# Kernel optimization log

Hardware: AMD Instinct MI355X
Metric: run time of the kernel (lower is better)

The kernel has to match this reference:

```python
import jax, jax.numpy as jnp
import numpy as np


def setup_inputs() -> dict:
    key = jax.random.key(0)
    k_x, k_wxh, k_whh, k_fcw, k_fcb = jax.random.split(key, 5)
    B, T, I, H = 256, 512, 64, 512
    x = jax.random.normal(k_x, (B, T, I), dtype=jnp.float32)
    W_xh = jax.random.normal(k_wxh, (I, H), dtype=jnp.float32) * 0.01
    W_hh = jax.random.normal(k_whh, (H, H), dtype=jnp.float32) * 0.01
    b = jnp.zeros((H,), dtype=jnp.float32)
    # nn.Linear(H, 1): weight (1, H), bias (1); init ~ U(-1/sqrt(H), 1/sqrt(H))
    lim = 1.0 / np.sqrt(H)
    fc_w = jax.random.uniform(k_fcw, (1, H), dtype=jnp.float32, minval=-lim, maxval=lim)
    fc_b = jax.random.uniform(k_fcb, (1,), dtype=jnp.float32, minval=-lim, maxval=lim)
    return {"x": x, "W_xh": W_xh, "W_hh": W_hh, "b": b, "fc_w": fc_w, "fc_b": fc_b}


def reference(x, W_xh, W_hh, b, fc_w, fc_b):
    B, T, I = x.shape
    H = W_hh.shape[0]
    # Precompute input projections for all timesteps in one big matmul: (B,T,H)
    xh = jnp.einsum('bti,ih->bth', x, W_xh) + b
    h0 = jnp.zeros((B, H), dtype=x.dtype)

    def step(h, xh_t):
        h_new = jnp.tanh(xh_t + h @ W_hh)
        return h_new, None

    h_final, _ = jax.lax.scan(step, h0, jnp.swapaxes(xh, 0, 1))  # scan over T
    return h_final @ fc_w.T + fc_b  # (B, 1)
```

## Files before the change

kernel.cpp:

```cpp
#include <hip/hip_runtime.h>


#define BATCH    256
#define TSTEPS   512
#define IDIM     64
#define HDIM     512
#define NTH      512

typedef _Float16 half2_t __attribute__((ext_vector_type(2)));
typedef _Float16 half8_t __attribute__((ext_vector_type(8)));

union H8U {
    half8_t v;
    half2_t p[4];
    uint4   u4;
};

__device__ __forceinline__ float fdot2(half2_t a, half2_t b, float c) {
#if __has_builtin(__builtin_amdgcn_fdot2)
    return __builtin_amdgcn_fdot2(a, b, c, false);
#else
    return c + (float)a[0] * (float)b[0] + (float)a[1] * (float)b[1];
#endif
}

__device__ __forceinline__ float fast_tanh(float x) {
    float e = __builtin_amdgcn_exp2f(x * 2.88539008177792681472f);
    return 1.0f - 2.0f * __builtin_amdgcn_rcpf(e + 1.0f);
}

#define XH_ROWS 16
__global__ __launch_bounds__(NTH, 4)
void xh_gemm(const float* __restrict__ x, const float* __restrict__ Wxh,
             const float* __restrict__ bias, _Float16* __restrict__ xh)
{
    const int j = threadIdx.x;
    const size_t r0 = (size_t)blockIdx.x * XH_ROWS;
    float wcol[IDIM];
#pragma unroll
    for (int i = 0; i < IDIM; ++i) wcol[i] = Wxh[(size_t)i * HDIM + j];
    const float bj = bias[j];
#pragma unroll
    for (int r = 0; r < XH_ROWS; ++r) {
        const float* xr = x + (r0 + r) * IDIM;
        float acc = bj;
#pragma unroll
        for (int i = 0; i < IDIM; ++i) acc += xr[i] * wcol[i];
        xh[(r0 + r) * HDIM + j] = (_Float16)acc;
    }
}

#define S_RP   192
#define S_RC   48
#define S_LC   16
#define S_LSTR 17
#define S_LDSW_BYTES (512 * S_LSTR * 16)
#define S_HBUF_OFF   S_LDSW_BYTES
#define S_HBUF_ELEMS 512
#define S_RED_OFF    (S_HBUF_OFF + 2 * S_HBUF_ELEMS * 2)
#define S_SMEM_BYTES (S_RED_OFF + 64)

__global__ __attribute__((amdgpu_flat_work_group_size(NTH, NTH), amdgpu_waves_per_eu(2, 2)))
void rnn_split(const _Float16* __restrict__ xh,
               const float* __restrict__ Whh,
               const float* __restrict__ fcw,
               const float* __restrict__ fcb,
               float* __restrict__ out)
{
    extern __shared__ char smem[];
    uint4*    ldsW = reinterpret_cast<uint4*>(smem);
    _Float16* hbuf = reinterpret_cast<_Float16*>(smem + S_HBUF_OFF);
    float*    red  = reinterpret_cast<float*>(smem + S_RED_OFF);

    const int j = threadIdx.x;
    const int b = blockIdx.x;

    half2_t wreg[S_RP];
#pragma unroll
    for (int p = 0; p < S_RP; ++p) {
        const int k = 2 * p;
        half2_t w;
        w[0] = (_Float16)Whh[(size_t)k * HDIM + j];
        w[1] = (_Float16)Whh[(size_t)(k + 1) * HDIM + j];
        wreg[p] = w;
    }
#pragma unroll
    for (int cc = 0; cc < S_LC; ++cc) {
        H8U u;
#pragma unroll
        for (int q = 0; q < 4; ++q) {
            const int k0 = 384 + 8 * cc + 2 * q;
            half2_t w;
            w[0] = (_Float16)Whh[(size_t)k0 * HDIM + j];
            w[1] = (_Float16)Whh[(size_t)(k0 + 1) * HDIM + j];
            u.p[q] = w;
        }
        ldsW[j * S_LSTR + cc] = u.u4;
    }

    const float fcwj = fcw[j];
    const _Float16* xhb = xh + (size_t)b * TSTEPS * HDIM;

    hbuf[j] = (_Float16)0.0f;
    __syncthreads();

    float hval = 0.0f;
    for (int t = 0; t < TSTEPS; ++t) {
        const int cur = t & 1;
        const int nxt = cur ^ 1;
        const _Float16* hb = hbuf + cur * S_HBUF_ELEMS;

        const float xv = (float)xhb[(size_t)t * HDIM + j];

        float a0 = 0.0f, a1 = 0.0f, a2 = 0.0f, a3 = 0.0f;
#pragma unroll
        for (int c = 0; c < S_RC; ++c) {
            H8U u;
            u.v = *reinterpret_cast<const half8_t*>(hb + 8 * c);
            a0 = fdot2(u.p[0], wreg[4 * c + 0], a0);
            a1 = fdot2(u.p[1], wreg[4 * c + 1], a1);
            a2 = fdot2(u.p[2], wreg[4 * c + 2], a2);
            a3 = fdot2(u.p[3], wreg[4 * c + 3], a3);
        }
#pragma unroll
        for (int cc = 0; cc < S_LC; ++cc) {
            H8U u, w;
            u.v  = *reinterpret_cast<const half8_t*>(hb + 8 * (S_RC + cc));
            w.u4 = ldsW[j * S_LSTR + cc];
            a0 = fdot2(u.p[0], w.p[0], a0);
            a1 = fdot2(u.p[1], w.p[1], a1);
            a2 = fdot2(u.p[2], w.p[2], a2);
            a3 = fdot2(u.p[3], w.p[3], a3);
        }
        hval = fast_tanh(((a0 + a1) + (a2 + a3)) + xv);

        hbuf[nxt * S_HBUF_ELEMS + j] = (_Float16)hval;
        __syncthreads();
    }

    float partial = hval * fcwj;
#pragma unroll
    for (int off = 32; off >= 1; off >>= 1)
        partial += __shfl_down(partial, off, 64);
    if ((j & 63) == 0) red[j >> 6] = partial;
    __syncthreads();
    if (j == 0) {
        float s = 0.0f;
#pragma unroll
        for (int w = 0; w < 8; ++w) s += red[w];
        out[b] = s + fcb[0];
    }
}

#define F_RP   216
#define F_RC   54
#define F_LC   18
#define F_LSTR 19
#define F_LDSW_BYTES (512 * F_LSTR * 16)
#define F_HBUF_OFF   F_LDSW_BYTES
#define F_HBUF_ELEMS 640
#define F_RED_OFF    (F_HBUF_OFF + 2 * F_HBUF_ELEMS * 2)
#define F_SMEM_BYTES (F_RED_OFF + 64)

__global__ __attribute__((amdgpu_flat_work_group_size(NTH, NTH), amdgpu_waves_per_eu(2, 2)))
void rnn_fused(const float* __restrict__ x, const float* __restrict__ Wxh,
               const float* __restrict__ Whh, const float* __restrict__ bias,
               const float* __restrict__ fcw, const float* __restrict__ fcb,
               float* __restrict__ out)
{
    extern __shared__ char smem[];
    uint4*    ldsW = reinterpret_cast<uint4*>(smem);
    _Float16* hbuf = reinterpret_cast<_Float16*>(smem + F_HBUF_OFF);
    float*    red  = reinterpret_cast<float*>(smem + F_RED_OFF);

    const int j = threadIdx.x;
    const int b = blockIdx.x;

    half2_t wreg[F_RP];
#pragma unroll
    for (int p = 0; p < F_RP; ++p) {
        const int k = 2 * p;
        half2_t w;
        w[0] = (_Float16)Whh[(size_t)k * HDIM + j];
        w[1] = (_Float16)Whh[(size_t)(k + 1) * HDIM + j];
        wreg[p] = w;
    }
#pragma unroll
    for (int cc = 0; cc < F_LC; ++cc) {
        H8U u;
#pragma unroll
        for (int q = 0; q < 4; ++q) {
            const int k0 = 432 + 8 * cc + 2 * q;
            const int k1 = k0 + 1;
            half2_t w;
            w[0] = (_Float16)(k0 < HDIM ? Whh[(size_t)k0 * HDIM + j]
                                        : Wxh[(size_t)(k0 - HDIM) * HDIM + j]);
            w[1] = (_Float16)(k1 < HDIM ? Whh[(size_t)k1 * HDIM + j]
                                        : Wxh[(size_t)(k1 - HDIM) * HDIM + j]);
            u.p[q] = w;
        }
        ldsW[j * F_LSTR + cc] = u.u4;
    }

    const float bj   = bias[j];
    const float fcwj = fcw[j];

    hbuf[j] = (_Float16)0.0f;
    if (j < IDIM) hbuf[HDIM + j] = (_Float16)x[((size_t)b * TSTEPS + 0) * IDIM + j];
    __syncthreads();

    float hval = 0.0f;
    for (int t = 0; t < TSTEPS; ++t) {
        const int cur = t & 1;
        const int nxt = cur ^ 1;
        const _Float16* hb = hbuf + cur * F_HBUF_ELEMS;

        float xv = 0.0f;
        const bool do_x = (j < IDIM) && (t + 1 < TSTEPS);
        if (do_x) xv = x[((size_t)b * TSTEPS + (t + 1)) * IDIM + j];

        float a0 = bj, a1 = 0.0f, a2 = 0.0f, a3 = 0.0f;
#pragma unroll
        for (int c = 0; c < F_RC; ++c) {
            H8U u;
            u.v = *reinterpret_cast<const half8_t*>(hb + 8 * c);
            a0 = fdot2(u.p[0], wreg[4 * c + 0], a0);
            a1 = fdot2(u.p[1], wreg[4 * c + 1], a1);
            a2 = fdot2(u.p[2], wreg[4 * c + 2], a2);
            a3 = fdot2(u.p[3], wreg[4 * c + 3], a3);
        }
#pragma unroll
        for (int cc = 0; cc < F_LC; ++cc) {
            H8U u, w;
            u.v  = *reinterpret_cast<const half8_t*>(hb + 8 * (F_RC + cc));
            w.u4 = ldsW[j * F_LSTR + cc];
            a0 = fdot2(u.p[0], w.p[0], a0);
            a1 = fdot2(u.p[1], w.p[1], a1);
            a2 = fdot2(u.p[2], w.p[2], a2);
            a3 = fdot2(u.p[3], w.p[3], a3);
        }
        hval = fast_tanh((a0 + a1) + (a2 + a3));

        hbuf[nxt * F_HBUF_ELEMS + j] = (_Float16)hval;
        if (do_x) hbuf[nxt * F_HBUF_ELEMS + HDIM + j] = (_Float16)xv;
        __syncthreads();
    }

    float partial = hval * fcwj;
#pragma unroll
    for (int off = 32; off >= 1; off >>= 1)
        partial += __shfl_down(partial, off, 64);
    if ((j & 63) == 0) red[j >> 6] = partial;
    __syncthreads();
    if (j == 0) {
        float s = 0.0f;
#pragma unroll
        for (int w = 0; w < 8; ++w) s += red[w];
        out[b] = s + fcb[0];
    }
}

extern "C" void kernel_launch(void* const* d_in, const int* in_sizes, int n_in,
                              void* d_out, int out_size, void* d_ws, size_t ws_size,
                              hipStream_t stream) {
    const float* x    = (const float*)d_in[0];
    const float* Wxh  = (const float*)d_in[1];
    const float* Whh  = (const float*)d_in[2];
    const float* bias = (const float*)d_in[3];
    const float* fcw  = (const float*)d_in[4];
    const float* fcb  = (const float*)d_in[5];
    float* out = (float*)d_out;

    const size_t xh_bytes = (size_t)BATCH * TSTEPS * HDIM * sizeof(_Float16);
    if (ws_size >= xh_bytes) {
        hipFuncSetAttribute(reinterpret_cast<const void*>(rnn_split),
                            hipFuncAttributeMaxDynamicSharedMemorySize, S_SMEM_BYTES);
        _Float16* xh = (_Float16*)d_ws;
        xh_gemm<<<(BATCH * TSTEPS) / XH_ROWS, NTH, 0, stream>>>(x, Wxh, bias, xh);
        rnn_split<<<BATCH, NTH, S_SMEM_BYTES, stream>>>(xh, Whh, fcw, fcb, out);
    } else {
        hipFuncSetAttribute(reinterpret_cast<const void*>(rnn_fused),
                            hipFuncAttributeMaxDynamicSharedMemorySize, F_SMEM_BYTES);
        rnn_fused<<<BATCH, NTH, F_SMEM_BYTES, stream>>>(x, Wxh, Whh, bias, fcw, fcb, out);
    }
}
```

Measured before the change: 1.189 ms.

## Split K across two thread halves and read h via scalar loads from a global ring

Replaces the separate xh GEMM plus recurrent kernel with a single 1024-thread kernel per batch row. The extended K (hidden state plus input) is split into two halves, one per 512-thread group, and partial sums are combined through LDS. The hidden state is stored in a per-batch ring buffer in global memory and read through readfirstlane-laundered constant-address-space pointers, so the loads become uniform scalar loads. This removes the xh intermediate and its traffic, and halves per-thread register weight storage. In exchange it adds a second barrier per step, and it relies on scalar-cache coherence for data written to global memory within the same kernel, which is risky.

```diff
diff --git a/kernel.cpp b/kernel.cpp
--- a/kernel.cpp
+++ b/kernel.cpp
@@ -5,10 +5,23 @@
 #define TSTEPS   512
 #define IDIM     64
 #define HDIM     512
-#define NTH      512
+#define KEXT     576
+#define KHALF    288
+#define NTH      1024
+#define RP       108
+#define LP       36
+#define LCH      9
+#define DEPTH    64
+#define ROWB     1152
+
+#define LDSW_BYTES (LCH * 16 * NTH)
+#define PSCR_OFF   LDSW_BYTES
+#define RED_OFF    (PSCR_OFF + HDIM * 4)
+#define SMEM_BYTES (RED_OFF + 64)
 
 typedef _Float16 half2_t __attribute__((ext_vector_type(2)));
 typedef _Float16 half8_t __attribute__((ext_vector_type(8)));
+typedef const __attribute__((address_space(4))) unsigned int* cu4p;
 
 union H8U {
     half8_t v;
@@ -29,129 +42,136 @@
     return 1.0f - 2.0f * __builtin_amdgcn_rcpf(e + 1.0f);
 }
 
-#define XH_ROWS 16
-__global__ __launch_bounds__(NTH, 4)
-void xh_gemm(const float* __restrict__ x, const float* __restrict__ Wxh,
-             const float* __restrict__ bias, _Float16* __restrict__ xh)
-{
-    const int j = threadIdx.x;
-    const size_t r0 = (size_t)blockIdx.x * XH_ROWS;
-    float wcol[IDIM];
-#pragma unroll
-    for (int i = 0; i < IDIM; ++i) wcol[i] = Wxh[(size_t)i * HDIM + j];
-    const float bj = bias[j];
-#pragma unroll
-    for (int r = 0; r < XH_ROWS; ++r) {
-        const float* xr = x + (r0 + r) * IDIM;
-        float acc = bj;
-#pragma unroll
-        for (int i = 0; i < IDIM; ++i) acc += xr[i] * wcol[i];
-        xh[(r0 + r) * HDIM + j] = (_Float16)acc;
-    }
-}
-
-#define S_RP   192
-#define S_RC   48
-#define S_LC   16
-#define S_LSTR 17
-#define S_LDSW_BYTES (512 * S_LSTR * 16)
-#define S_HBUF_OFF   S_LDSW_BYTES
-#define S_HBUF_ELEMS 512
-#define S_RED_OFF    (S_HBUF_OFF + 2 * S_HBUF_ELEMS * 2)
-#define S_SMEM_BYTES (S_RED_OFF + 64)
-
-__global__ __attribute__((amdgpu_flat_work_group_size(NTH, NTH), amdgpu_waves_per_eu(2, 2)))
-void rnn_split(const _Float16* __restrict__ xh,
-               const float* __restrict__ Whh,
-               const float* __restrict__ fcw,
-               const float* __restrict__ fcb,
-               float* __restrict__ out)
+__device__ __forceinline__ float ldW(const float* __restrict__ Whh,
+                                     const float* __restrict__ Wxh, int k, int j) {
+    return k < HDIM ? Whh[(size_t)k * HDIM + j] : Wxh[(size_t)(k - HDIM) * HDIM + j];
+}
+
+__device__ __forceinline__ half2_t bc_h2(unsigned int u) {
+    union { unsigned int u; half2_t h; } c;
+    c.u = u;
+    return c.h;
+}
+
+__global__ __launch_bounds__(NTH)
+void rnn_smem(const float* __restrict__ x,
+              const float* __restrict__ Wxh,
+              const float* __restrict__ Whh,
+              const float* __restrict__ bias,
+              const float* __restrict__ fcw,
+              const float* __restrict__ fcb,
+              _Float16* __restrict__ hring,
+              float* __restrict__ out)
 {
     extern __shared__ char smem[];
-    uint4*    ldsW = reinterpret_cast<uint4*>(smem);
-    _Float16* hbuf = reinterpret_cast<_Float16*>(smem + S_HBUF_OFF);
-    float*    red  = reinterpret_cast<float*>(smem + S_RED_OFF);
-
-    const int j = threadIdx.x;
-    const int b = blockIdx.x;
-
-    half2_t wreg[S_RP];
-#pragma unroll
-    for (int p = 0; p < S_RP; ++p) {
-        const int k = 2 * p;
+    uint4* ldsW = reinterpret_cast<uint4*>(smem);
+    float* pscr = reinterpret_cast<float*>(smem + PSCR_OFF);
+    float* red  = reinterpret_cast<float*>(smem + RED_OFF);
+
+    const int tid = threadIdx.x;
+    const int kh  = tid >> 9;
+    const int j   = tid & (HDIM - 1);
+    const int b   = blockIdx.x;
+    const int khm = kh * KHALF;
+
+    half2_t wreg[RP];
+#pragma unroll
+    for (int p = 0; p < RP; ++p) {
+        const int k = khm + 2 * p;
         half2_t w;
-        w[0] = (_Float16)Whh[(size_t)k * HDIM + j];
-        w[1] = (_Float16)Whh[(size_t)(k + 1) * HDIM + j];
+        w[0] = (_Float16)ldW(Whh, Wxh, k, j);
+        w[1] = (_Float16)ldW(Whh, Wxh, k + 1, j);
         wreg[p] = w;
     }
 #pragma unroll
-    for (int cc = 0; cc < S_LC; ++cc) {
+    for (int c = 0; c < LCH; ++c) {
         H8U u;
 #pragma unroll
         for (int q = 0; q < 4; ++q) {
-            const int k0 = 384 + 8 * cc + 2 * q;
+            const int m = RP + 4 * c + q;
+            const int k = khm + 2 * m;
             half2_t w;
-            w[0] = (_Float16)Whh[(size_t)k0 * HDIM + j];
-            w[1] = (_Float16)Whh[(size_t)(k0 + 1) * HDIM + j];
+            w[0] = (_Float16)ldW(Whh, Wxh, k, j);
+            w[1] = (_Float16)ldW(Whh, Wxh, k + 1, j);
             u.p[q] = w;
         }
-        ldsW[j * S_LSTR + cc] = u.u4;
-    }
-
+        ldsW[c * NTH + tid] = u.u4;
+    }
+
+    const float bj   = bias[j];
     const float fcwj = fcw[j];
-    const _Float16* xhb = xh + (size_t)b * TSTEPS * HDIM;
-
-    hbuf[j] = (_Float16)0.0f;
+
+    _Float16* hrows = hring + (size_t)b * DEPTH * KEXT;
+
+    if (!kh) {
+        hrows[j] = (_Float16)0.0f;
+    } else if (j < IDIM) {
+        hrows[HDIM + j] = (_Float16)x[((size_t)b * TSTEPS + 0) * IDIM + j];
+    }
     __syncthreads();
+
+    const uintptr_t praw = (uintptr_t)hrows + (size_t)khm * 2;
 
     float hval = 0.0f;
     for (int t = 0; t < TSTEPS; ++t) {
-        const int cur = t & 1;
-        const int nxt = cur ^ 1;
-        const _Float16* hb = hbuf + cur * S_HBUF_ELEMS;
-
-        const float xv = (float)xhb[(size_t)t * HDIM + j];
+        unsigned int lo = __builtin_amdgcn_readfirstlane((unsigned int)praw);
+        unsigned int hi = __builtin_amdgcn_readfirstlane((unsigned int)(praw >> 32));
+        const uintptr_t laund = ((uintptr_t)hi << 32) | (uintptr_t)lo;
+        cu4p hrow = (cu4p)(laund + (size_t)(t & (DEPTH - 1)) * ROWB);
+
+        float xnext = 0.0f;
+        const bool dox = kh && (j < IDIM) && (t + 1 < TSTEPS);
+        if (dox) xnext = x[((size_t)b * TSTEPS + (t + 1)) * IDIM + j];
 
         float a0 = 0.0f, a1 = 0.0f, a2 = 0.0f, a3 = 0.0f;
 #pragma unroll
-        for (int c = 0; c < S_RC; ++c) {
-            H8U u;
-            u.v = *reinterpret_cast<const half8_t*>(hb + 8 * c);
-            a0 = fdot2(u.p[0], wreg[4 * c + 0], a0);
-            a1 = fdot2(u.p[1], wreg[4 * c + 1], a1);
-            a2 = fdot2(u.p[2], wreg[4 * c + 2], a2);
-            a3 = fdot2(u.p[3], wreg[4 * c + 3], a3);
-        }
-#pragma unroll
-        for (int cc = 0; cc < S_LC; ++cc) {
-            H8U u, w;
-            u.v  = *reinterpret_cast<const half8_t*>(hb + 8 * (S_RC + cc));
-            w.u4 = ldsW[j * S_LSTR + cc];
-            a0 = fdot2(u.p[0], w.p[0], a0);
-            a1 = fdot2(u.p[1], w.p[1], a1);
-            a2 = fdot2(u.p[2], w.p[2], a2);
-            a3 = fdot2(u.p[3], w.p[3], a3);
-        }
-        hval = fast_tanh(((a0 + a1) + (a2 + a3)) + xv);
-
-        hbuf[nxt * S_HBUF_ELEMS + j] = (_Float16)hval;
+        for (int p = 0; p < RP; p += 4) {
+            a0 = fdot2(bc_h2(hrow[p + 0]), wreg[p + 0], a0);
+            a1 = fdot2(bc_h2(hrow[p + 1]), wreg[p + 1], a1);
+            a2 = fdot2(bc_h2(hrow[p + 2]), wreg[p + 2], a2);
+            a3 = fdot2(bc_h2(hrow[p + 3]), wreg[p + 3], a3);
+        }
+#pragma unroll
+        for (int c = 0; c < LCH; ++c) {
+            const uint4 wv = ldsW[c * NTH + tid];
+            const int m = RP + 4 * c;
+            a0 = fdot2(bc_h2(hrow[m + 0]), bc_h2(wv.x), a0);
+            a1 = fdot2(bc_h2(hrow[m + 1]), bc_h2(wv.y), a1);
+            a2 = fdot2(bc_h2(hrow[m + 2]), bc_h2(wv.z), a2);
+            a3 = fdot2(bc_h2(hrow[m + 3]), bc_h2(wv.w), a3);
+        }
+        const float aa = (a0 + a1) + (a2 + a3);
+
+        if (kh) pscr[j] = aa;
         __syncthreads();
-    }
-
-    float partial = hval * fcwj;
+
+        const int nslot = (t + 1) & (DEPTH - 1);
+        if (!kh) {
+            const float tot = aa + pscr[j] + bj;
+            hval = fast_tanh(tot);
+            if (t + 1 < TSTEPS)
+                hrows[(size_t)nslot * KEXT + j] = (_Float16)hval;
+        } else if (dox) {
+            hrows[(size_t)nslot * KEXT + HDIM + j] = (_Float16)xnext;
+        }
+        __syncthreads();
+    }
+
+    float partial = (!kh) ? hval * fcwj : 0.0f;
 #pragma unroll
     for (int off = 32; off >= 1; off >>= 1)
         partial += __shfl_down(partial, off, 64);
-    if ((j & 63) == 0) red[j >> 6] = partial;
+    if ((tid & 63) == 0) red[tid >> 6] = partial;
     __syncthreads();
-    if (j == 0) {
+    if (tid == 0) {
         float s = 0.0f;
 #pragma unroll
-        for (int w = 0; w < 8; ++w) s += red[w];
+        for (int w = 0; w < 16; ++w) s += red[w];
         out[b] = s + fcb[0];
     }
 }
 
+#define F_NTH  512
 #define F_RP   216
 #define F_RC   54
 #define F_LC   18
@@ -162,7 +182,7 @@
 #define F_RED_OFF    (F_HBUF_OFF + 2 * F_HBUF_ELEMS * 2)
 #define F_SMEM_BYTES (F_RED_OFF + 64)
 
-__global__ __attribute__((amdgpu_flat_work_group_size(NTH, NTH), amdgpu_waves_per_eu(2, 2)))
+__global__ __attribute__((amdgpu_flat_work_group_size(F_NTH, F_NTH), amdgpu_waves_per_eu(2, 2)))
 void rnn_fused(const float* __restrict__ x, const float* __restrict__ Wxh,
                const float* __restrict__ Whh, const float* __restrict__ bias,
                const float* __restrict__ fcw, const float* __restrict__ fcb,
@@ -191,12 +211,9 @@
 #pragma unroll
         for (int q = 0; q < 4; ++q) {
             const int k0 = 432 + 8 * cc + 2 * q;
-            const int k1 = k0 + 1;
             half2_t w;
-            w[0] = (_Float16)(k0 < HDIM ? Whh[(size_t)k0 * HDIM + j]
-                                        : Wxh[(size_t)(k0 - HDIM) * HDIM + j]);
-            w[1] = (_Float16)(k1 < HDIM ? Whh[(size_t)k1 * HDIM + j]
-                                        : Wxh[(size_t)(k1 - HDIM) * HDIM + j]);
+            w[0] = (_Float16)ldW(Whh, Wxh, k0, j);
+            w[1] = (_Float16)ldW(Whh, Wxh, k0 + 1, j);
             u.p[q] = w;
         }
         ldsW[j * F_LSTR + cc] = u.u4;
@@ -271,16 +288,15 @@
     const float* fcb  = (const float*)d_in[5];
     float* out = (float*)d_out;
 
-    const size_t xh_bytes = (size_t)BATCH * TSTEPS * HDIM * sizeof(_Float16);
-    if (ws_size >= xh_bytes) {
-        hipFuncSetAttribute(reinterpret_cast<const void*>(rnn_split),
-                            hipFuncAttributeMaxDynamicSharedMemorySize, S_SMEM_BYTES);
-        _Float16* xh = (_Float16*)d_ws;
-        xh_gemm<<<(BATCH * TSTEPS) / XH_ROWS, NTH, 0, stream>>>(x, Wxh, bias, xh);
-        rnn_split<<<BATCH, NTH, S_SMEM_BYTES, stream>>>(xh, Whh, fcw, fcb, out);
+    const size_t ring_bytes = (size_t)BATCH * DEPTH * ROWB;
+    if (ws_size >= ring_bytes) {
+        hipFuncSetAttribute(reinterpret_cast<const void*>(rnn_smem),
+                            hipFuncAttributeMaxDynamicSharedMemorySize, SMEM_BYTES);
+        _Float16* hring = (_Float16*)d_ws;
+        rnn_smem<<<BATCH, NTH, SMEM_BYTES, stream>>>(x, Wxh, Whh, bias, fcw, fcb, hring, out);
     } else {
         hipFuncSetAttribute(reinterpret_cast<const void*>(rnn_fused),
                             hipFuncAttributeMaxDynamicSharedMemorySize, F_SMEM_BYTES);
-        rnn_fused<<<BATCH, NTH, F_SMEM_BYTES, stream>>>(x, Wxh, Whh, bias, fcw, fcb, out);
-    }
-}
+        rnn_fused<<<BATCH, F_NTH, F_SMEM_BYTES, stream>>>(x, Wxh, Whh, bias, fcw, fcb, out);
+    }
+}
```

Measured after the change: 1.436 ms. 1.21x slower.

## Replace per-thread fdot2 recurrence with MFMA 16x16x32 matrix ops

Applied to the files above, without the earlier changes.

The recurrent matvec in the split path now uses MFMA f16 instructions. The h vector is broadcast as the A operand, and W_hh is laid out in per-wave B fragments: 12 k-tiles are kept in registers and 4 are staged in LDS. Each wave covers 64 output columns across 4 n-tiles, and only row 0 of each 16x16 result is used. This aims to replace the long serial fdot2 chains per thread with matrix-core throughput. In exchange, 15 of the 16 A rows are wasted compute, and only 16 lanes per wave do the tanh and write-back.

```diff
diff --git a/kernel.cpp b/kernel.cpp
--- a/kernel.cpp
+++ b/kernel.cpp
@@ -6,23 +6,27 @@
 #define IDIM     64
 #define HDIM     512
 #define NTH      512
-
-typedef _Float16 half2_t __attribute__((ext_vector_type(2)));
-typedef _Float16 half8_t __attribute__((ext_vector_type(8)));
+#define WAVES    8
+#define NT       4
+#define RKT      12
+#define LKT      4
+#define KT       16
+
+#define LDSW_BYTES (WAVES * NT * LKT * 64 * 16)
+#define HB_OFF     LDSW_BYTES
+#define RED_OFF    (HB_OFF + 2 * HDIM * 2)
+#define SMEM_BYTES (RED_OFF + 64)
+
+typedef _Float16 half2_t  __attribute__((ext_vector_type(2)));
+typedef _Float16 half8_t  __attribute__((ext_vector_type(8)));
+typedef float    float4_t __attribute__((ext_vector_type(4)));
 
 union H8U {
-    half8_t v;
-    half2_t p[4];
-    uint4   u4;
+    half8_t  v;
+    half2_t  p[4];
+    uint4    u4;
+    _Float16 e[8];
 };
-
-__device__ __forceinline__ float fdot2(half2_t a, half2_t b, float c) {
-#if __has_builtin(__builtin_amdgcn_fdot2)
-    return __builtin_amdgcn_fdot2(a, b, c, false);
-#else
-    return c + (float)a[0] * (float)b[0] + (float)a[1] * (float)b[1];
-#endif
-}
 
 __device__ __forceinline__ float fast_tanh(float x) {
     float e = __builtin_amdgcn_exp2f(x * 2.88539008177792681472f);
@@ -50,104 +54,114 @@
     }
 }
 
-#define S_RP   192
-#define S_RC   48
-#define S_LC   16
-#define S_LSTR 17
-#define S_LDSW_BYTES (512 * S_LSTR * 16)
-#define S_HBUF_OFF   S_LDSW_BYTES
-#define S_HBUF_ELEMS 512
-#define S_RED_OFF    (S_HBUF_OFF + 2 * S_HBUF_ELEMS * 2)
-#define S_SMEM_BYTES (S_RED_OFF + 64)
-
 __global__ __attribute__((amdgpu_flat_work_group_size(NTH, NTH), amdgpu_waves_per_eu(2, 2)))
-void rnn_split(const _Float16* __restrict__ xh,
-               const float* __restrict__ Whh,
-               const float* __restrict__ fcw,
-               const float* __restrict__ fcb,
-               float* __restrict__ out)
+void rnn_mfma(const _Float16* __restrict__ xh,
+              const float* __restrict__ Whh,
+              const float* __restrict__ fcw,
+              const float* __restrict__ fcb,
+              float* __restrict__ out)
 {
     extern __shared__ char smem[];
-    uint4*    ldsW = reinterpret_cast<uint4*>(smem);
-    _Float16* hbuf = reinterpret_cast<_Float16*>(smem + S_HBUF_OFF);
-    float*    red  = reinterpret_cast<float*>(smem + S_RED_OFF);
-
-    const int j = threadIdx.x;
-    const int b = blockIdx.x;
-
-    half2_t wreg[S_RP];
-#pragma unroll
-    for (int p = 0; p < S_RP; ++p) {
-        const int k = 2 * p;
-        half2_t w;
-        w[0] = (_Float16)Whh[(size_t)k * HDIM + j];
-        w[1] = (_Float16)Whh[(size_t)(k + 1) * HDIM + j];
-        wreg[p] = w;
-    }
-#pragma unroll
-    for (int cc = 0; cc < S_LC; ++cc) {
-        H8U u;
-#pragma unroll
-        for (int q = 0; q < 4; ++q) {
-            const int k0 = 384 + 8 * cc + 2 * q;
-            half2_t w;
-            w[0] = (_Float16)Whh[(size_t)k0 * HDIM + j];
-            w[1] = (_Float16)Whh[(size_t)(k0 + 1) * HDIM + j];
-            u.p[q] = w;
-        }
-        ldsW[j * S_LSTR + cc] = u.u4;
-    }
-
-    const float fcwj = fcw[j];
-    const _Float16* xhb = xh + (size_t)b * TSTEPS * HDIM;
-
-    hbuf[j] = (_Float16)0.0f;
+    char*     ldsW = smem;
+    _Float16* hb   = reinterpret_cast<_Float16*>(smem + HB_OFF);
+    float*    red  = reinterpret_cast<float*>(smem + RED_OFF);
+
+    const int tid  = threadIdx.x;
+    const int w    = tid >> 6;
+    const int lane = tid & 63;
+    const int l15  = lane & 15;
+    const int quad = lane >> 4;
+    const int b    = blockIdx.x;
+
+    half8_t breg[NT][RKT];
+#pragma unroll
+    for (int nt = 0; nt < NT; ++nt) {
+        const int col = 64 * w + 16 * nt + l15;
+#pragma unroll
+        for (int kt = 0; kt < KT; ++kt) {
+            const int k0 = 32 * kt + quad * 8;
+            H8U u;
+#pragma unroll
+            for (int jj = 0; jj < 8; ++jj)
+                u.e[jj] = (_Float16)Whh[(size_t)(k0 + jj) * HDIM + col];
+            if (kt < RKT) {
+                breg[nt][kt] = u.v;
+            } else {
+                *reinterpret_cast<uint4*>(
+                    ldsW + (size_t)(((w * NT + nt) * LKT + (kt - RKT)) * 64 + lane) * 16) = u.u4;
+            }
+        }
+    }
+
+    hb[tid] = (_Float16)0.0f;
     __syncthreads();
 
-    float hval = 0.0f;
+    const _Float16* xhrow = xh + (size_t)b * TSTEPS * HDIM;
+
+    float hout[NT] = {0.f, 0.f, 0.f, 0.f};
     for (int t = 0; t < TSTEPS; ++t) {
         const int cur = t & 1;
         const int nxt = cur ^ 1;
-        const _Float16* hb = hbuf + cur * S_HBUF_ELEMS;
-
-        const float xv = (float)xhb[(size_t)t * HDIM + j];
-
-        float a0 = 0.0f, a1 = 0.0f, a2 = 0.0f, a3 = 0.0f;
-#pragma unroll
-        for (int c = 0; c < S_RC; ++c) {
-            H8U u;
-            u.v = *reinterpret_cast<const half8_t*>(hb + 8 * c);
-            a0 = fdot2(u.p[0], wreg[4 * c + 0], a0);
-            a1 = fdot2(u.p[1], wreg[4 * c + 1], a1);
-            a2 = fdot2(u.p[2], wreg[4 * c + 2], a2);
-            a3 = fdot2(u.p[3], wreg[4 * c + 3], a3);
-        }
-#pragma unroll
-        for (int cc = 0; cc < S_LC; ++cc) {
-            H8U u, w;
-            u.v  = *reinterpret_cast<const half8_t*>(hb + 8 * (S_RC + cc));
-            w.u4 = ldsW[j * S_LSTR + cc];
-            a0 = fdot2(u.p[0], w.p[0], a0);
-            a1 = fdot2(u.p[1], w.p[1], a1);
-            a2 = fdot2(u.p[2], w.p[2], a2);
-            a3 = fdot2(u.p[3], w.p[3], a3);
-        }
-        hval = fast_tanh(((a0 + a1) + (a2 + a3)) + xv);
-
-        hbuf[nxt * S_HBUF_ELEMS + j] = (_Float16)hval;
+
+        _Float16 xv[NT];
+#pragma unroll
+        for (int nt = 0; nt < NT; ++nt)
+            xv[nt] = xhrow[t * HDIM + 64 * w + 16 * nt + l15];
+
+        float4_t acc[NT];
+#pragma unroll
+        for (int nt = 0; nt < NT; ++nt) acc[nt] = (float4_t){0.f, 0.f, 0.f, 0.f};
+
+        const char* abase = smem + HB_OFF + cur * 1024 + quad * 16;
+
+#pragma unroll
+        for (int kt = 0; kt < RKT; ++kt) {
+            H8U a;
+            a.u4 = *reinterpret_cast<const uint4*>(abase + kt * 64);
+#pragma unroll
+            for (int nt = 0; nt < NT; ++nt)
+                acc[nt] = __builtin_amdgcn_mfma_f32_16x16x32_f16(a.v, breg[nt][kt], acc[nt], 0, 0, 0);
+        }
+#pragma unroll
+        for (int ktl = 0; ktl < LKT; ++ktl) {
+            H8U a;
+            a.u4 = *reinterpret_cast<const uint4*>(abase + (RKT + ktl) * 64);
+#pragma unroll
+            for (int nt = 0; nt < NT; ++nt) {
+                H8U bb;
+                bb.u4 = *reinterpret_cast<const uint4*>(
+                    ldsW + (size_t)(((w * NT + nt) * LKT + ktl) * 64 + lane) * 16);
+                acc[nt] = __builtin_amdgcn_mfma_f32_16x16x32_f16(a.v, bb.v, acc[nt], 0, 0, 0);
+            }
+        }
+
+#pragma unroll
+        for (int nt = 0; nt < NT; ++nt)
+            hout[nt] = fast_tanh(acc[nt][0] + (float)xv[nt]);
+
+        if (lane < 16) {
+#pragma unroll
+            for (int nt = 0; nt < NT; ++nt)
+                hb[nxt * HDIM + 64 * w + 16 * nt + lane] = (_Float16)hout[nt];
+        }
         __syncthreads();
     }
 
-    float partial = hval * fcwj;
+    float partial = 0.0f;
+    if (lane < 16) {
+#pragma unroll
+        for (int nt = 0; nt < NT; ++nt)
+            partial += hout[nt] * fcw[64 * w + 16 * nt + lane];
+    }
 #pragma unroll
     for (int off = 32; off >= 1; off >>= 1)
         partial += __shfl_down(partial, off, 64);
-    if ((j & 63) == 0) red[j >> 6] = partial;
+    if (lane == 0) red[w] = partial;
     __syncthreads();
-    if (j == 0) {
+    if (tid == 0) {
         float s = 0.0f;
 #pragma unroll
-        for (int w = 0; w < 8; ++w) s += red[w];
+        for (int i = 0; i < WAVES; ++i) s += red[i];
         out[b] = s + fcb[0];
     }
 }
@@ -161,6 +175,19 @@
 #define F_HBUF_ELEMS 640
 #define F_RED_OFF    (F_HBUF_OFF + 2 * F_HBUF_ELEMS * 2)
 #define F_SMEM_BYTES (F_RED_OFF + 64)
+
+__device__ __forceinline__ float fdot2(half2_t a, half2_t b, float c) {
+#if __has_builtin(__builtin_amdgcn_fdot2)
+    return __builtin_amdgcn_fdot2(a, b, c, false);
+#else
+    return c + (float)a[0] * (float)b[0] + (float)a[1] * (float)b[1];
+#endif
+}
+
+__device__ __forceinline__ float ldW(const float* __restrict__ Whh,
+                                     const float* __restrict__ Wxh, int k, int j) {
+    return k < HDIM ? Whh[(size_t)k * HDIM + j] : Wxh[(size_t)(k - HDIM) * HDIM + j];
+}
 
 __global__ __attribute__((amdgpu_flat_work_group_size(NTH, NTH), amdgpu_waves_per_eu(2, 2)))
 void rnn_fused(const float* __restrict__ x, const float* __restrict__ Wxh,
@@ -191,12 +218,9 @@
 #pragma unroll
         for (int q = 0; q < 4; ++q) {
             const int k0 = 432 + 8 * cc + 2 * q;
-            const int k1 = k0 + 1;
             half2_t w;
-            w[0] = (_Float16)(k0 < HDIM ? Whh[(size_t)k0 * HDIM + j]
-                                        : Wxh[(size_t)(k0 - HDIM) * HDIM + j]);
-            w[1] = (_Float16)(k1 < HDIM ? Whh[(size_t)k1 * HDIM + j]
-                                        : Wxh[(size_t)(k1 - HDIM) * HDIM + j]);
+            w[0] = (_Float16)ldW(Whh, Wxh, k0, j);
+            w[1] = (_Float16)ldW(Whh, Wxh, k0 + 1, j);
             u.p[q] = w;
         }
         ldsW[j * F_LSTR + cc] = u.u4;
@@ -213,17 +237,17 @@
     for (int t = 0; t < TSTEPS; ++t) {
         const int cur = t & 1;
         const int nxt = cur ^ 1;
-        const _Float16* hb = hbuf + cur * F_HBUF_ELEMS;
-
-        float xv = 0.0f;
+        const _Float16* hbp = hbuf + cur * F_HBUF_ELEMS;
+
+        float xvv = 0.0f;
         const bool do_x = (j < IDIM) && (t + 1 < TSTEPS);
-        if (do_x) xv = x[((size_t)b * TSTEPS + (t + 1)) * IDIM + j];
+        if (do_x) xvv = x[((size_t)b * TSTEPS + (t + 1)) * IDIM + j];
 
         float a0 = bj, a1 = 0.0f, a2 = 0.0f, a3 = 0.0f;
 #pragma unroll
         for (int c = 0; c < F_RC; ++c) {
             H8U u;
-            u.v = *reinterpret_cast<const half8_t*>(hb + 8 * c);
+            u.v = *reinterpret_cast<const half8_t*>(hbp + 8 * c);
             a0 = fdot2(u.p[0], wreg[4 * c + 0], a0);
             a1 = fdot2(u.p[1], wreg[4 * c + 1], a1);
             a2 = fdot2(u.p[2], wreg[4 * c + 2], a2);
@@ -231,18 +255,18 @@
         }
 #pragma unroll
         for (int cc = 0; cc < F_LC; ++cc) {
-            H8U u, w;
-            u.v  = *reinterpret_cast<const half8_t*>(hb + 8 * (F_RC + cc));
-            w.u4 = ldsW[j * F_LSTR + cc];
-            a0 = fdot2(u.p[0], w.p[0], a0);
-            a1 = fdot2(u.p[1], w.p[1], a1);
-            a2 = fdot2(u.p[2], w.p[2], a2);
-            a3 = fdot2(u.p[3], w.p[3], a3);
+            H8U u, wv;
+            u.v   = *reinterpret_cast<const half8_t*>(hbp + 8 * (F_RC + cc));
+            wv.u4 = ldsW[j * F_LSTR + cc];
+            a0 = fdot2(u.p[0], wv.p[0], a0);
+            a1 = fdot2(u.p[1], wv.p[1], a1);
+            a2 = fdot2(u.p[2], wv.p[2], a2);
+            a3 = fdot2(u.p[3], wv.p[3], a3);
         }
         hval = fast_tanh((a0 + a1) + (a2 + a3));
 
         hbuf[nxt * F_HBUF_ELEMS + j] = (_Float16)hval;
-        if (do_x) hbuf[nxt * F_HBUF_ELEMS + HDIM + j] = (_Float16)xv;
+        if (do_x) hbuf[nxt * F_HBUF_ELEMS + HDIM + j] = (_Float16)xvv;
         __syncthreads();
     }
 
@@ -255,7 +279,7 @@
     if (j == 0) {
         float s = 0.0f;
 #pragma unroll
-        for (int w = 0; w < 8; ++w) s += red[w];
+        for (int wv = 0; wv < 8; ++wv) s += red[wv];
         out[b] = s + fcb[0];
     }
 }
@@ -273,11 +297,11 @@
 
     const size_t xh_bytes = (size_t)BATCH * TSTEPS * HDIM * sizeof(_Float16);
     if (ws_size >= xh_bytes) {
-        hipFuncSetAttribute(reinterpret_cast<const void*>(rnn_split),
-                            hipFuncAttributeMaxDynamicSharedMemorySize, S_SMEM_BYTES);
+        hipFuncSetAttribute(reinterpret_cast<const void*>(rnn_mfma),
+                            hipFuncAttributeMaxDynamicSharedMemorySize, SMEM_BYTES);
         _Float16* xh = (_Float16*)d_ws;
         xh_gemm<<<(BATCH * TSTEPS) / XH_ROWS, NTH, 0, stream>>>(x, Wxh, bias, xh);
-        rnn_split<<<BATCH, NTH, S_SMEM_BYTES, stream>>>(xh, Whh, fcw, fcb, out);
+        rnn_mfma<<<BATCH, NTH, SMEM_BYTES, stream>>>(xh, Whh, fcw, fcb, out);
     } else {
         hipFuncSetAttribute(reinterpret_cast<const void*>(rnn_fused),
                             hipFuncAttributeMaxDynamicSharedMemorySize, F_SMEM_BYTES);
```

Measured after the change: 1.242 ms. +4.5%, slower.
